# Optimization experiments

Measured on AMD Instinct MI355X. Metric: run time of the kernel, lower is better.

The kernel has to match this reference:

```python
import jax, jax.numpy as jnp
import numpy as np

TEMPERATURE = 0.5  # set externally on the torch module; fixed here
EPS = 1e-10

B, NPTS, NDIM = 8, 1024, 64
K, S = 16, 512  # n_clusters, book_size


def setup_inputs() -> dict:
    key = jax.random.key(0)
    k1, k2, k3, k4 = jax.random.split(key, 4)
    ze = jax.random.normal(k1, (B, NPTS, NDIM), dtype=jnp.float32)
    # per-sample cluster probabilities (rows sum to 1)
    c_probs = jax.nn.softmax(jax.random.normal(k2, (B, K), dtype=jnp.float32), axis=-1)
    books = jax.random.normal(k3, (K, S, NDIM), dtype=jnp.float32)
    log_param_q = jnp.asarray(np.log(1.0), dtype=jnp.float32)  # param_q_init = 1.0
    gumbel_u = jax.random.uniform(k4, (B, K, NPTS, S), dtype=jnp.float32)
    return {"ze": ze, "c_probs": c_probs, "books": books,
            "log_param_q": log_param_q, "gumbel_u": gumbel_u}


def reference(ze, c_probs, books, log_param_q, gumbel_u):
    # precision of the Gaussian quantizer
    precision_q = 0.5 / jnp.clip(jnp.exp(log_param_q), 1e-10)
    # squared euclidean distances: [b, k, n, s]
    d = (jnp.sum(ze * ze, axis=-1)[:, None, :, None]
         + jnp.sum(books * books, axis=-1)[None, :, None, :]
         - 2.0 * jnp.einsum('bnd,ksd->bkns', ze, books))
    logits = -d * precision_q                                   # [b,k,n,s]
    # gumbel-softmax sample (training branch)
    g = -jnp.log(-jnp.log(gumbel_u + EPS) + EPS)
    encodings = jax.nn.softmax((logits + g) / TEMPERATURE, axis=-1)
    # soft codebook lookup, mixed over clusters by per-sample c_probs
    zq = jnp.einsum('bkns,ksd,bk->bnd', encodings, books, c_probs)
    prob = jax.nn.softmax(logits, axis=-1)
    log_prob = jax.nn.log_softmax(logits, axis=-1)
    return (zq, precision_q, prob, log_prob)
```

## Files before the change

kernel.cpp:

```cpp
#include <hip/hip_runtime.h>
#include <hip/hip_bf16.h>

typedef __attribute__((ext_vector_type(8))) short short8;
typedef __attribute__((ext_vector_type(4))) float f32x4;
typedef __attribute__((ext_vector_type(2))) float f32x2;

#define WS_ZE     0u
#define WS_ZELO   (1u<<20)
#define WS_B1H    (2u<<20)
#define WS_B1L    (3u<<20)
#define WS_B2     (4u<<20)
#define WS_ZN2    (5u<<20)
#define WS_BS2    ((5u<<20)+32768u)
#define WS_ZQP    (6u<<20)

__device__ __forceinline__ unsigned short f2bf(float x) {
  __hip_bfloat16 h = __float2bfloat16(x);
  return __builtin_bit_cast(unsigned short, h);
}
__device__ __forceinline__ float bf2f(unsigned short u) {
  union { unsigned int i; float f; } x; x.i = ((unsigned int)u) << 16; return x.f;
}
__device__ __forceinline__ void lds_barrier() {
  asm volatile("s_waitcnt lgkmcnt(0)" ::: "memory");
  __builtin_amdgcn_s_barrier();
}

__global__ __launch_bounds__(256) void prep_ze_k(const float* __restrict__ ze,
                                                 char* __restrict__ ws) {
  int t = blockIdx.x * 256 + threadIdx.x;
  if (t >= 8 * 1024) return;
  const f32x4* row = (const f32x4*)(ze + t * 64);
  unsigned short* dh = (unsigned short*)(ws + WS_ZE) + t * 64;
  unsigned short* dl = (unsigned short*)(ws + WS_ZELO) + t * 64;
  float s = 0.f;
#pragma unroll
  for (int c = 0; c < 8; ++c) {
    const f32x4 v0 = row[2 * c], v1 = row[2 * c + 1];
    union { unsigned short u[8]; short8 v; } H, L;
#pragma unroll
    for (int r = 0; r < 4; ++r) {
      float a = v0[r]; s += a * a;
      unsigned short h = f2bf(a); H.u[r] = h; L.u[r] = f2bf(a - bf2f(h));
      float b = v1[r]; s += b * b;
      unsigned short h2 = f2bf(b); H.u[4 + r] = h2; L.u[4 + r] = f2bf(b - bf2f(h2));
    }
    *(short8*)(dh + c * 8) = H.v;
    *(short8*)(dl + c * 8) = L.v;
  }
  ((float*)(ws + WS_ZN2))[t] = s;
}

__global__ __launch_bounds__(256) void prep_bnorm_k(const float* __restrict__ books,
                                                    const float* __restrict__ lpq,
                                                    char* __restrict__ ws,
                                                    float* __restrict__ d_out) {
  int t = blockIdx.x * 256 + threadIdx.x;
  if (t == 0) d_out[524288] = 0.5f / fmaxf(expf(lpq[0]), 1e-10f);
  if (t >= 16 * 512) return;
  const f32x4* row = (const f32x4*)(books + t * 64);
  float s = 0.f;
#pragma unroll
  for (int c = 0; c < 16; ++c) {
    const f32x4 v = row[c];
#pragma unroll
    for (int r = 0; r < 4; ++r) s += v[r] * v[r];
  }
  ((float*)(ws + WS_BS2))[t] = s;
}

__global__ __launch_bounds__(256) void prep_b1_k(const float* __restrict__ books,
                                                 char* __restrict__ ws) {
  int t = blockIdx.x * 256 + threadIdx.x;
  const int sl = t & 15, g = (t >> 4) & 3, f = (t >> 6) & 1, tt = (t >> 7) & 31, k = t >> 12;
  const float* src = books + ((k * 512 + tt * 16 + sl) * 64 + f * 32 + g * 8);
  const f32x4 v0 = *(const f32x4*)(src);
  const f32x4 v1 = *(const f32x4*)(src + 4);
  union { unsigned short u[8]; short8 v; } H, L;
#pragma unroll
  for (int r = 0; r < 4; ++r) {
    unsigned short h = f2bf(v0[r]); H.u[r] = h; L.u[r] = f2bf(v0[r] - bf2f(h));
    unsigned short h2 = f2bf(v1[r]); H.u[4 + r] = h2; L.u[4 + r] = f2bf(v1[r] - bf2f(h2));
  }
  const int off = (k * 32 + tt) * 2048 + f * 1024 + (sl + g * 16) * 16;
  *(short8*)(ws + WS_B1H + off) = H.v;
  *(short8*)(ws + WS_B1L + off) = L.v;
}

__global__ __launch_bounds__(256) void prep_b2_k(const float* __restrict__ books,
                                                 char* __restrict__ ws) {
  int t = blockIdx.x * 256 + threadIdx.x;
  const int l15 = t & 15, sub = (t >> 4) & 3, m = (t >> 6) & 3, w = (t >> 8) & 7,
            hh = (t >> 11) & 1, k = t >> 12;
  const float* src = books + ((k * 512 + hh * 256 + w * 32 + sub * 8) * 64 + m * 16 + l15);
  union { unsigned short u[8]; short8 v; } H;
#pragma unroll
  for (int j = 0; j < 8; ++j) H.u[j] = f2bf(src[j * 64]);
  *(short8*)(ws + WS_B2 + k * 65536 + ((hh * 8 + w) * 4 + m) * 1024 + (l15 + sub * 16) * 16) = H.v;
}

__global__ __launch_bounds__(256) void zq_red_k(const char* __restrict__ ws,
                                                float* __restrict__ d_out) {
  int t = blockIdx.x * 256 + threadIdx.x;
  const f32x4 a = *(const f32x4*)(ws + WS_ZQP + t * 16);
  const f32x4 b = *(const f32x4*)(ws + WS_ZQP + (1u << 21) + t * 16);
  *(f32x4*)(d_out + t * 4) = a + b;
}

__global__ __launch_bounds__(512, 3)
void gvq_main(const float* __restrict__ gum, const float* __restrict__ cprobs,
              const float* __restrict__ lpq, char* __restrict__ ws,
              float* __restrict__ d_out) {
  __shared__ char lds[50240];
  char* lgb  = lds;
  char* encb = lds + 33024;
  float* scr_esc = (float*)(lds + 50176);

  const int tid  = threadIdx.x;
  const int lane = tid & 63;
  const int wave = tid >> 6;
  const int l15  = lane & 15;
  const int g4   = lane >> 4;

  const int bid = blockIdx.x;
  const int kg  = bid & 1;
  const int bt  = bid >> 1;
  const int b   = bt >> 6;
  const int n0  = (bt & 63) * 16;

  const float prec  = 0.5f / fmaxf(expf(lpq[0]), 1e-10f);
  const float prec2 = 2.0f * prec;
  const float C24   = 3.7751345442790977e-11f;

  const unsigned short* zh = (const unsigned short*)(ws + WS_ZE)   + (b * 1024 + n0 + l15) * 64;
  const unsigned short* zl = (const unsigned short*)(ws + WS_ZELO) + (b * 1024 + n0 + l15) * 64;
  const short8 zf0h = *(const short8*)(zh + g4 * 8);
  const short8 zf1h = *(const short8*)(zh + 32 + g4 * 8);
  const short8 zf0l = *(const short8*)(zl + g4 * 8);
  const short8 zf1l = *(const short8*)(zl + 32 + g4 * 8);
  const float zn2p = ((const float*)(ws + WS_ZN2))[b * 1024 + n0 + l15] * prec;

  f32x4 zacc[4] = {{0,0,0,0},{0,0,0,0},{0,0,0,0},{0,0,0,0}};

  const int nr0 = wave * 2, nr1 = wave * 2 + 1;

#pragma unroll 1
  for (int kk = 0; kk < 8; ++kk) {
    const int k = kg * 8 + kk;
    const float cp = cprobs[b * 16 + k];
    const char* b1h = ws + WS_B1H + k * 65536;
    const char* b1l = ws + WS_B1L + k * 65536;
    const char* b2  = ws + WS_B2  + k * 65536;
    const float* bs2k = (const float*)(ws + WS_BS2) + k * 512;
    const long row0 = ((long)((b * 16 + k) * 1024) + n0 + nr0) * 512;
    const long row1 = ((long)((b * 16 + k) * 1024) + n0 + nr1) * 512;

#pragma unroll
    for (int i = 0; i < 4; ++i) {
      const int t = wave * 4 + i;
      const char* bh = b1h + t * 2048 + lane * 16;
      const char* bl = b1l + t * 2048 + lane * 16;
      const short8 a0h = *(const short8*)(bh);
      const short8 a1h = *(const short8*)(bh + 1024);
      const short8 a0l = *(const short8*)(bl);
      const short8 a1l = *(const short8*)(bl + 1024);
      f32x4 c = {0.f, 0.f, 0.f, 0.f};
      c = __builtin_amdgcn_mfma_f32_16x16x32_bf16(a0h, zf0h, c, 0, 0, 0);
      c = __builtin_amdgcn_mfma_f32_16x16x32_bf16(a1h, zf1h, c, 0, 0, 0);
      c = __builtin_amdgcn_mfma_f32_16x16x32_bf16(a0h, zf0l, c, 0, 0, 0);
      c = __builtin_amdgcn_mfma_f32_16x16x32_bf16(a1h, zf1l, c, 0, 0, 0);
      c = __builtin_amdgcn_mfma_f32_16x16x32_bf16(a0l, zf0h, c, 0, 0, 0);
      c = __builtin_amdgcn_mfma_f32_16x16x32_bf16(a1l, zf1h, c, 0, 0, 0);
      const f32x4 bs2v = *(const f32x4*)(bs2k + t * 16 + g4 * 4);
      f32x4 lv;
#pragma unroll
      for (int r = 0; r < 4; ++r)
        lv[r] = fmaf(c[r], prec2, fmaf(bs2v[r], -prec, -zn2p));
      *(f32x4*)(lgb + l15 * 2064 + (t * 16 + g4 * 4) * 4) = lv;
    }

    float uv0[8], uv1[8];
#pragma unroll
    for (int j = 0; j < 8; ++j)
      uv0[j] = __builtin_nontemporal_load(gum + row0 + j * 64 + lane);
#pragma unroll
    for (int j = 0; j < 8; ++j)
      uv1[j] = __builtin_nontemporal_load(gum + row1 + j * 64 + lane);

    lds_barrier();

#pragma unroll
    for (int r = 0; r < 2; ++r) {
      const int n = r ? nr1 : nr0;
      const long rowb = r ? row1 : row0;
      float Lv[8], e1[8];
      const float* l32 = (const float*)(lgb + n * 2064);
#pragma unroll
      for (int j = 0; j < 8; ++j) Lv[j] = l32[j * 64 + lane];

      float m = Lv[0];
#pragma unroll
      for (int j = 1; j < 8; ++j) m = fmaxf(m, Lv[j]);
#pragma unroll
      for (int o = 1; o < 64; o <<= 1) m = fmaxf(m, __shfl_xor(m, o));

      unsigned short* er = (unsigned short*)(encb + n * 1072);
      float z1 = 0.f, z2 = 0.f;
#pragma unroll
      for (int j = 0; j < 8; ++j) {
        const float u = r ? uv1[j] : uv0[j];
        e1[j] = __expf(Lv[j] - m); z1 += e1[j];
        const float L  = 1e-10f - __logf(u + 1e-10f);
        const float rl = __builtin_amdgcn_rcpf(L);
        const float e2 = (e1[j] * e1[j]) * (rl * rl) * C24;
        z2 += e2;
        er[j * 64 + lane] = f2bf(e2);
      }
#pragma unroll
      for (int o = 1; o < 64; o <<= 1) {
        z1 += __shfl_xor(z1, o);
        z2 += __shfl_xor(z2, o);
      }
      const float rz1 = 1.0f / z1;
      const float c1  = m + __logf(z1);
      if (lane == 0) scr_esc[n] = cp / z2;

      float* pp = d_out + 524289 + rowb;
      float* pl = pp + 67108864;
#pragma unroll
      for (int j = 0; j < 8; ++j)
        __builtin_nontemporal_store(e1[j] * rz1, pp + j * 64 + lane);
#pragma unroll
      for (int j = 0; j < 8; ++j)
        __builtin_nontemporal_store(Lv[j] - c1, pl + j * 64 + lane);
    }
    lds_barrier();

    {
      f32x4 cacc[4] = {{0,0,0,0},{0,0,0,0},{0,0,0,0},{0,0,0,0}};
#pragma unroll
      for (int h = 0; h < 2; ++h) {
        const short8 bf = *(const short8*)(encb + l15 * 1072 +
                                           (h * 256 + wave * 32 + g4 * 8) * 2);
        const char* afb = b2 + ((h * 8 + wave) * 4) * 1024 + lane * 16;
#pragma unroll
        for (int m = 0; m < 4; ++m) {
          const short8 af = *(const short8*)(afb + m * 1024);
          cacc[m] = __builtin_amdgcn_mfma_f32_16x16x32_bf16(af, bf, cacc[m], 0, 0, 0);
        }
      }
      const float esc = scr_esc[l15];
#pragma unroll
      for (int m = 0; m < 4; ++m)
#pragma unroll
        for (int r = 0; r < 4; ++r) zacc[m][r] = fmaf(cacc[m][r], esc, zacc[m][r]);
    }
  }

  __syncthreads();
#pragma unroll
  for (int m = 0; m < 4; ++m)
    *(f32x4*)(lds + wave * 4096 + l15 * 256 + m * 64 + g4 * 16) = zacc[m];
  __syncthreads();
  const int e = tid * 2;
  f32x2 acc = {0.f, 0.f};
#pragma unroll
  for (int w = 0; w < 8; ++w) acc += *(const f32x2*)(lds + w * 4096 + e * 4);
  *(f32x2*)(ws + WS_ZQP + (unsigned)kg * (1u << 21) +
            (((unsigned)(b * 1024 + n0)) * 64 + e) * 4) = acc;
}

extern "C" void kernel_launch(void* const* d_in, const int* in_sizes, int n_in,
                              void* d_out, int out_size, void* d_ws, size_t ws_size,
                              hipStream_t stream) {
  (void)in_sizes; (void)n_in; (void)out_size; (void)ws_size;
  const float* ze     = (const float*)d_in[0];
  const float* cprobs = (const float*)d_in[1];
  const float* books  = (const float*)d_in[2];
  const float* lpq    = (const float*)d_in[3];
  const float* gum    = (const float*)d_in[4];
  float* out = (float*)d_out;
  char* ws = (char*)d_ws;
  hipLaunchKernelGGL(prep_ze_k,    dim3(32),   dim3(256), 0, stream, ze, ws);
  hipLaunchKernelGGL(prep_bnorm_k, dim3(32),   dim3(256), 0, stream, books, lpq, ws, out);
  hipLaunchKernelGGL(prep_b1_k,    dim3(256),  dim3(256), 0, stream, books, ws);
  hipLaunchKernelGGL(prep_b2_k,    dim3(256),  dim3(256), 0, stream, books, ws);
  hipLaunchKernelGGL(gvq_main,     dim3(1024), dim3(512), 0, stream, gum, cprobs, lpq, ws, out);
  hipLaunchKernelGGL(zq_red_k,     dim3(512),  dim3(256), 0, stream, ws, out);
}
```

Before: 236.7 us.

## Fuse prep kernels into one launch and split clusters three ways across blocks

Merges the four preprocessing kernels into a single launch that dispatches on block index. The main kernel's cluster dimension now splits into three groups (6/5/5) instead of two, giving 1536 blocks instead of 1024, which better fills the CUs given 3 blocks per CU. The reduction kernel sums three partial zq buffers instead of two. The cost is an uneven per-block workload and extra partial-buffer traffic.

```diff
diff --git a/kernel.cpp b/kernel.cpp
--- a/kernel.cpp
+++ b/kernel.cpp
@@ -26,85 +26,79 @@
   __builtin_amdgcn_s_barrier();
 }
 
-__global__ __launch_bounds__(256) void prep_ze_k(const float* __restrict__ ze,
-                                                 char* __restrict__ ws) {
-  int t = blockIdx.x * 256 + threadIdx.x;
-  if (t >= 8 * 1024) return;
-  const f32x4* row = (const f32x4*)(ze + t * 64);
-  unsigned short* dh = (unsigned short*)(ws + WS_ZE) + t * 64;
-  unsigned short* dl = (unsigned short*)(ws + WS_ZELO) + t * 64;
-  float s = 0.f;
-#pragma unroll
-  for (int c = 0; c < 8; ++c) {
-    const f32x4 v0 = row[2 * c], v1 = row[2 * c + 1];
+__global__ __launch_bounds__(256) void prep_all_k(const float* __restrict__ ze,
+                                                  const float* __restrict__ books,
+                                                  const float* __restrict__ lpq,
+                                                  char* __restrict__ ws,
+                                                  float* __restrict__ d_out) {
+  const int bb = blockIdx.x;
+  if (bb < 32) {
+    int t = bb * 256 + threadIdx.x;
+    const f32x4* row = (const f32x4*)(ze + t * 64);
+    unsigned short* dh = (unsigned short*)(ws + WS_ZE) + t * 64;
+    unsigned short* dl = (unsigned short*)(ws + WS_ZELO) + t * 64;
+    float s = 0.f;
+#pragma unroll
+    for (int c = 0; c < 8; ++c) {
+      const f32x4 v0 = row[2 * c], v1 = row[2 * c + 1];
+      union { unsigned short u[8]; short8 v; } H, L;
+#pragma unroll
+      for (int r = 0; r < 4; ++r) {
+        float a = v0[r]; s += a * a;
+        unsigned short h = f2bf(a); H.u[r] = h; L.u[r] = f2bf(a - bf2f(h));
+        float b = v1[r]; s += b * b;
+        unsigned short h2 = f2bf(b); H.u[4 + r] = h2; L.u[4 + r] = f2bf(b - bf2f(h2));
+      }
+      *(short8*)(dh + c * 8) = H.v;
+      *(short8*)(dl + c * 8) = L.v;
+    }
+    ((float*)(ws + WS_ZN2))[t] = s;
+  } else if (bb < 64) {
+    int t = (bb - 32) * 256 + threadIdx.x;
+    if (t == 0) d_out[524288] = 0.5f / fmaxf(expf(lpq[0]), 1e-10f);
+    const f32x4* row = (const f32x4*)(books + t * 64);
+    float s = 0.f;
+#pragma unroll
+    for (int c = 0; c < 16; ++c) {
+      const f32x4 v = row[c];
+#pragma unroll
+      for (int r = 0; r < 4; ++r) s += v[r] * v[r];
+    }
+    ((float*)(ws + WS_BS2))[t] = s;
+  } else if (bb < 320) {
+    int t = (bb - 64) * 256 + threadIdx.x;
+    const int sl = t & 15, g = (t >> 4) & 3, f = (t >> 6) & 1, tt = (t >> 7) & 31, k = t >> 12;
+    const float* src = books + ((k * 512 + tt * 16 + sl) * 64 + f * 32 + g * 8);
+    const f32x4 v0 = *(const f32x4*)(src);
+    const f32x4 v1 = *(const f32x4*)(src + 4);
     union { unsigned short u[8]; short8 v; } H, L;
 #pragma unroll
     for (int r = 0; r < 4; ++r) {
-      float a = v0[r]; s += a * a;
-      unsigned short h = f2bf(a); H.u[r] = h; L.u[r] = f2bf(a - bf2f(h));
-      float b = v1[r]; s += b * b;
-      unsigned short h2 = f2bf(b); H.u[4 + r] = h2; L.u[4 + r] = f2bf(b - bf2f(h2));
-    }
-    *(short8*)(dh + c * 8) = H.v;
-    *(short8*)(dl + c * 8) = L.v;
+      unsigned short h = f2bf(v0[r]); H.u[r] = h; L.u[r] = f2bf(v0[r] - bf2f(h));
+      unsigned short h2 = f2bf(v1[r]); H.u[4 + r] = h2; L.u[4 + r] = f2bf(v1[r] - bf2f(h2));
+    }
+    const int off = (k * 32 + tt) * 2048 + f * 1024 + (sl + g * 16) * 16;
+    *(short8*)(ws + WS_B1H + off) = H.v;
+    *(short8*)(ws + WS_B1L + off) = L.v;
+  } else {
+    int t = (bb - 320) * 256 + threadIdx.x;
+    const int l15 = t & 15, sub = (t >> 4) & 3, m = (t >> 6) & 3, w = (t >> 8) & 7,
+              hh = (t >> 11) & 1, k = t >> 12;
+    const float* src = books + ((k * 512 + hh * 256 + w * 32 + sub * 8) * 64 + m * 16 + l15);
+    union { unsigned short u[8]; short8 v; } H;
+#pragma unroll
+    for (int j = 0; j < 8; ++j) H.u[j] = f2bf(src[j * 64]);
+    *(short8*)(ws + WS_B2 + k * 65536 + ((hh * 8 + w) * 4 + m) * 1024 + (l15 + sub * 16) * 16) = H.v;
   }
-  ((float*)(ws + WS_ZN2))[t] = s;
-}
-
-__global__ __launch_bounds__(256) void prep_bnorm_k(const float* __restrict__ books,
-                                                    const float* __restrict__ lpq,
-                                                    char* __restrict__ ws,
-                                                    float* __restrict__ d_out) {
-  int t = blockIdx.x * 256 + threadIdx.x;
-  if (t == 0) d_out[524288] = 0.5f / fmaxf(expf(lpq[0]), 1e-10f);
-  if (t >= 16 * 512) return;
-  const f32x4* row = (const f32x4*)(books + t * 64);
-  float s = 0.f;
-#pragma unroll
-  for (int c = 0; c < 16; ++c) {
-    const f32x4 v = row[c];
-#pragma unroll
-    for (int r = 0; r < 4; ++r) s += v[r] * v[r];
-  }
-  ((float*)(ws + WS_BS2))[t] = s;
-}
-
-__global__ __launch_bounds__(256) void prep_b1_k(const float* __restrict__ books,
-                                                 char* __restrict__ ws) {
-  int t = blockIdx.x * 256 + threadIdx.x;
-  const int sl = t & 15, g = (t >> 4) & 3, f = (t >> 6) & 1, tt = (t >> 7) & 31, k = t >> 12;
-  const float* src = books + ((k * 512 + tt * 16 + sl) * 64 + f * 32 + g * 8);
-  const f32x4 v0 = *(const f32x4*)(src);
-  const f32x4 v1 = *(const f32x4*)(src + 4);
-  union { unsigned short u[8]; short8 v; } H, L;
-#pragma unroll
-  for (int r = 0; r < 4; ++r) {
-    unsigned short h = f2bf(v0[r]); H.u[r] = h; L.u[r] = f2bf(v0[r] - bf2f(h));
-    unsigned short h2 = f2bf(v1[r]); H.u[4 + r] = h2; L.u[4 + r] = f2bf(v1[r] - bf2f(h2));
-  }
-  const int off = (k * 32 + tt) * 2048 + f * 1024 + (sl + g * 16) * 16;
-  *(short8*)(ws + WS_B1H + off) = H.v;
-  *(short8*)(ws + WS_B1L + off) = L.v;
-}
-
-__global__ __launch_bounds__(256) void prep_b2_k(const float* __restrict__ books,
-                                                 char* __restrict__ ws) {
-  int t = blockIdx.x * 256 + threadIdx.x;
-  const int l15 = t & 15, sub = (t >> 4) & 3, m = (t >> 6) & 3, w = (t >> 8) & 7,
-            hh = (t >> 11) & 1, k = t >> 12;
-  const float* src = books + ((k * 512 + hh * 256 + w * 32 + sub * 8) * 64 + m * 16 + l15);
-  union { unsigned short u[8]; short8 v; } H;
-#pragma unroll
-  for (int j = 0; j < 8; ++j) H.u[j] = f2bf(src[j * 64]);
-  *(short8*)(ws + WS_B2 + k * 65536 + ((hh * 8 + w) * 4 + m) * 1024 + (l15 + sub * 16) * 16) = H.v;
 }
 
 __global__ __launch_bounds__(256) void zq_red_k(const char* __restrict__ ws,
                                                 float* __restrict__ d_out) {
   int t = blockIdx.x * 256 + threadIdx.x;
   const f32x4 a = *(const f32x4*)(ws + WS_ZQP + t * 16);
-  const f32x4 b = *(const f32x4*)(ws + WS_ZQP + (1u << 21) + t * 16);
-  *(f32x4*)(d_out + t * 4) = a + b;
+  const f32x4 b = *(const f32x4*)(ws + WS_ZQP + (2u << 20) + t * 16);
+  const f32x4 c = *(const f32x4*)(ws + WS_ZQP + (4u << 20) + t * 16);
+  *(f32x4*)(d_out + t * 4) = a + b + c;
 }
 
 __global__ __launch_bounds__(512, 3)
@@ -123,10 +117,12 @@
   const int g4   = lane >> 4;
 
   const int bid = blockIdx.x;
-  const int kg  = bid & 1;
-  const int bt  = bid >> 1;
+  const unsigned kg = (unsigned)bid % 3u;
+  const int bt  = (int)((unsigned)bid / 3u);
   const int b   = bt >> 6;
   const int n0  = (bt & 63) * 16;
+  const int kbeg = (kg == 0) ? 0 : (kg == 1 ? 6 : 11);
+  const int kcnt = (kg == 0) ? 6 : 5;
 
   const float prec  = 0.5f / fmaxf(expf(lpq[0]), 1e-10f);
   const float prec2 = 2.0f * prec;
@@ -145,8 +141,8 @@
   const int nr0 = wave * 2, nr1 = wave * 2 + 1;
 
 #pragma unroll 1
-  for (int kk = 0; kk < 8; ++kk) {
-    const int k = kg * 8 + kk;
+  for (int kk = 0; kk < kcnt; ++kk) {
+    const int k = kbeg + kk;
     const float cp = cprobs[b * 16 + k];
     const char* b1h = ws + WS_B1H + k * 65536;
     const char* b1l = ws + WS_B1L + k * 65536;
@@ -266,7 +262,7 @@
   f32x2 acc = {0.f, 0.f};
 #pragma unroll
   for (int w = 0; w < 8; ++w) acc += *(const f32x2*)(lds + w * 4096 + e * 4);
-  *(f32x2*)(ws + WS_ZQP + (unsigned)kg * (1u << 21) +
+  *(f32x2*)(ws + WS_ZQP + kg * (2u << 20) +
             (((unsigned)(b * 1024 + n0)) * 64 + e) * 4) = acc;
 }
 
@@ -281,10 +277,7 @@
   const float* gum    = (const float*)d_in[4];
   float* out = (float*)d_out;
   char* ws = (char*)d_ws;
-  hipLaunchKernelGGL(prep_ze_k,    dim3(32),   dim3(256), 0, stream, ze, ws);
-  hipLaunchKernelGGL(prep_bnorm_k, dim3(32),   dim3(256), 0, stream, books, lpq, ws, out);
-  hipLaunchKernelGGL(prep_b1_k,    dim3(256),  dim3(256), 0, stream, books, ws);
-  hipLaunchKernelGGL(prep_b2_k,    dim3(256),  dim3(256), 0, stream, books, ws);
-  hipLaunchKernelGGL(gvq_main,     dim3(1024), dim3(512), 0, stream, gum, cprobs, lpq, ws, out);
-  hipLaunchKernelGGL(zq_red_k,     dim3(512),  dim3(256), 0, stream, ws, out);
-}
+  hipLaunchKernelGGL(prep_all_k, dim3(576),  dim3(256), 0, stream, ze, books, lpq, ws, out);
+  hipLaunchKernelGGL(gvq_main,   dim3(1536), dim3(512), 0, stream, gum, cprobs, lpq, ws, out);
+  hipLaunchKernelGGL(zq_red_k,   dim3(512),  dim3(256), 0, stream, ws, out);
+}
```

Measured after the change: 233.1 us. No clear change (-1.5%).
